# Performance work log

Measured on AMD Instinct MI355X. Metric: run time of the kernel, lower is better.

## Reference

```python
import jax, jax.numpy as jnp
import numpy as np

NUM_GRAPHS = 1024


def setup_inputs() -> dict:
    key = jax.random.key(0)
    k1, k2, k3, k4 = jax.random.split(key, 4)
    N, D = 1000000, 128
    node_embeddings = jax.random.normal(k1, (N, D), dtype=jnp.float32)
    batch_idx = jnp.sort(jax.random.randint(k2, (N,), 0, NUM_GRAPHS))
    # gate MLP params (Linear(D,D) -> ReLU -> Linear(D,1)), scaled like kaiming-ish init
    W1 = jax.random.normal(k3, (D, D), dtype=jnp.float32) / np.sqrt(D)
    b1 = jnp.zeros((D,), dtype=jnp.float32)
    W2 = jax.random.normal(k4, (D, 1), dtype=jnp.float32) / np.sqrt(D)
    b2 = jnp.zeros((1,), dtype=jnp.float32)
    return {"node_embeddings": node_embeddings, "batch_idx": batch_idx,
            "W1": W1, "b1": b1, "W2": W2, "b2": b2}


def reference(node_embeddings, batch_idx, W1, b1, W2, b2):
    # gate = sigmoid(Linear(ReLU(Linear(x))))  -> [N, 1]
    h = jax.nn.relu(node_embeddings @ W1 + b1)          # [N, D]
    gate = jax.nn.sigmoid(h @ W2 + b2)                   # [N, 1]
    gated = gate * node_embeddings                       # [N, D]
    # scatter-sum over batch_idx -> per-graph embedding [B, D]
    graph_embedding = jax.ops.segment_sum(gated, batch_idx, num_segments=NUM_GRAPHS)
    return graph_embedding
```

## Files before the change

### kernel.cpp

```cpp
#include <hip/hip_runtime.h>
#include <stdint.h>

#define D 128
#define TM 64
#define GRID 768
#define NTHREADS 256
#define PPS 17

typedef float f32x4 __attribute__((ext_vector_type(4)));
typedef short s16x8 __attribute__((ext_vector_type(8)));
typedef uint32_t u32x2 __attribute__((ext_vector_type(2)));

__device__ __forceinline__ uint32_t f2bf_u(float f) {
    union { float f; uint32_t u; } v; v.f = f;
    return (v.u + 0x7fffu + ((v.u >> 16) & 1u)) >> 16;
}
__device__ __forceinline__ short f2bf(float f) { return (short)f2bf_u(f); }
__device__ __forceinline__ uint32_t cvt_pk_bf16(float lo, float hi) {
    uint32_t r;
    asm("v_cvt_pk_bf16_f32 %0, %1, %2" : "=v"(r) : "v"(lo), "v"(hi));
    return r;
}

__global__ __launch_bounds__(NTHREADS, 3)
void gate_agg_kernel(const float* __restrict__ X,
                     const int* __restrict__ bidx,
                     const float* __restrict__ W1,
                     const float* __restrict__ b1,
                     const float* __restrict__ W2,
                     const float* __restrict__ b2,
                     float* __restrict__ out,
                     int NT)
{
    __shared__ short xtile[TM * D];
    __shared__ float pp[64 * PPS];
    __shared__ u32x2 gidL[TM];
    __shared__ int   idxL[TM];

    const int tid = threadIdx.x;
    const int l = tid & 63;
    const int w = tid >> 6;
    const int l15 = l & 15;
    const int lk = l >> 4;

    s16x8 bfr[2][4];
    #pragma unroll
    for (int j = 0; j < 2; ++j) {
        const int n = (2 * w + j) * 16 + l15;
        #pragma unroll
        for (int kt = 0; kt < 4; ++kt) {
            #pragma unroll
            for (int e = 0; e < 8; ++e)
                bfr[j][kt][e] = f2bf(W1[(kt * 32 + lk * 8 + e) * D + n]);
        }
    }
    float b1v[2], w2v[2];
    #pragma unroll
    for (int j = 0; j < 2; ++j) {
        b1v[j] = b1[(2 * w + j) * 16 + l15];
        w2v[j] = W2[(2 * w + j) * 16 + l15];
    }
    const float b2s = b2[0];

    const int q = NT / GRID, rem = NT % GRID;
    int t0, t1;
    if ((int)blockIdx.x < rem) { t0 = blockIdx.x * (q + 1); t1 = t0 + q + 1; }
    else { t0 = rem * (q + 1) + ((int)blockIdx.x - rem) * q; t1 = t0 + q; }

    const int cc = tid & 31;
    const int rg = tid >> 5;
    float acc3[4] = {0.f, 0.f, 0.f, 0.f};
    int cur = -1;

    f32x4 v[8];
    int ridx = 0;
    if (t0 < t1) {
        const float* xg = X + (size_t)t0 * TM * D;
        #pragma unroll
        for (int j = 0; j < 8; ++j)
            v[j] = *(const f32x4*)(xg + (size_t)(j * 256 + tid) * 4);
        if (tid < TM) ridx = bidx[(size_t)t0 * TM + tid];
    }

    for (int t = t0; t < t1; ++t) {
        #pragma unroll
        for (int j = 0; j < 8; ++j) {
            int qc = j * 256 + tid;
            int row = qc >> 5, cq = qc & 31;
            int c2 = cq >> 1, h = cq & 1;
            u32x2 wv;
            wv[0] = cvt_pk_bf16(v[j][0], v[j][1]);
            wv[1] = cvt_pk_bf16(v[j][2], v[j][3]);
            *(u32x2*)((char*)xtile + row * 256 + ((c2 ^ (row & 15)) << 4) + h * 8) = wv;
        }
        if (tid < TM) idxL[tid] = ridx;
        __syncthreads();

        if (t + 1 < t1) {
            const float* xg = X + (size_t)(t + 1) * TM * D;
            #pragma unroll
            for (int j = 0; j < 8; ++j)
                v[j] = *(const f32x4*)(xg + (size_t)(j * 256 + tid) * 4);
            if (tid < TM) ridx = bidx[(size_t)(t + 1) * TM + tid];
        }

        f32x4 acc[4][2];
        #pragma unroll
        for (int rf = 0; rf < 4; ++rf) { acc[rf][0] = (f32x4)0.f; acc[rf][1] = (f32x4)0.f; }

        #pragma unroll
        for (int kt = 0; kt < 4; ++kt) {
            const int kc = kt * 4 + lk;
            #pragma unroll
            for (int rf = 0; rf < 4; ++rf) {
                const int R = rf * 16 + l15;
                s16x8 a = *(const s16x8*)((const char*)xtile + R * 256 + ((kc ^ l15) << 4));
                acc[rf][0] = __builtin_amdgcn_mfma_f32_16x16x32_bf16(a, bfr[0][kt], acc[rf][0], 0, 0, 0);
                acc[rf][1] = __builtin_amdgcn_mfma_f32_16x16x32_bf16(a, bfr[1][kt], acc[rf][1], 0, 0, 0);
            }
        }

        #pragma unroll
        for (int rf = 0; rf < 4; ++rf) {
            float pr[4];
            #pragma unroll
            for (int r = 0; r < 4; ++r) {
                float s = 0.f;
                #pragma unroll
                for (int j = 0; j < 2; ++j) {
                    float h = acc[rf][j][r] + b1v[j];
                    h = fmaxf(h, 0.f);
                    s = fmaf(h, w2v[j], s);
                }
                s += __shfl_xor(s, 1, 64);
                s += __shfl_xor(s, 2, 64);
                pr[r] = s;
            }
            float val = pr[0];
            val = ((l & 3) == 1) ? pr[1] : val;
            val = ((l & 3) == 2) ? pr[2] : val;
            val = ((l & 3) == 3) ? pr[3] : val;
            pp[(rf * 16 + lk * 4 + (l & 3)) * PPS + w * 4 + ((l >> 2) & 3)] = val;
        }
        __syncthreads();

        if (tid < TM) {
            float s = 0.f;
            #pragma unroll
            for (int c = 0; c < 16; ++c) s += pp[tid * PPS + c];
            float g = 1.f / (1.f + __expf(-(s + b2s)));
            u32x2 gi; gi[0] = __float_as_uint(g); gi[1] = (uint32_t)idxL[tid];
            gidL[tid] = gi;
        }
        __syncthreads();

        #pragma unroll
        for (int rr = 0; rr < 8; ++rr) {
            int r = rg * 8 + rr;
            u32x2 gi = gidL[r];
            int seg = (int)gi[1];
            float g = __uint_as_float(gi[0]);
            if (seg != cur) {
                if (cur >= 0) {
                    #pragma unroll
                    for (int i = 0; i < 4; ++i)
                        atomicAdd(out + (size_t)cur * D + 4 * cc + i, acc3[i]);
                }
                acc3[0] = acc3[1] = acc3[2] = acc3[3] = 0.f;
                cur = seg;
            }
            u32x2 xw = *(const u32x2*)((const char*)xtile + r * 256 +
                        (((cc >> 1) ^ (r & 15)) << 4) + (cc & 1) * 8);
            float f0 = __uint_as_float(xw[0] << 16);
            float f1 = __uint_as_float(xw[0] & 0xffff0000u);
            float f2 = __uint_as_float(xw[1] << 16);
            float f3 = __uint_as_float(xw[1] & 0xffff0000u);
            acc3[0] = fmaf(g, f0, acc3[0]);
            acc3[1] = fmaf(g, f1, acc3[1]);
            acc3[2] = fmaf(g, f2, acc3[2]);
            acc3[3] = fmaf(g, f3, acc3[3]);
        }
        __syncthreads();
    }
    if (cur >= 0) {
        #pragma unroll
        for (int i = 0; i < 4; ++i)
            atomicAdd(out + (size_t)cur * D + 4 * cc + i, acc3[i]);
    }
}

extern "C" void kernel_launch(void* const* d_in, const int* in_sizes, int n_in,
                              void* d_out, int out_size, void* d_ws, size_t ws_size,
                              hipStream_t stream) {
    const float* X    = (const float*)d_in[0];
    const int*   bidx = (const int*)d_in[1];
    const float* W1   = (const float*)d_in[2];
    const float* b1   = (const float*)d_in[3];
    const float* W2   = (const float*)d_in[4];
    const float* b2   = (const float*)d_in[5];
    float* out = (float*)d_out;

    const int N  = in_sizes[0] / D;
    const int NT = N / TM;

    hipMemsetAsync(d_out, 0, (size_t)out_size * sizeof(float), stream);
    gate_agg_kernel<<<GRID, NTHREADS, 0, stream>>>(X, bidx, W1, b1, W2, b2, out, NT);
}
```

Baseline: 122.0 us.

## Stream fp32 tiles into double-buffered LDS via direct global-to-LDS loads

Replaces the register-staged prefetch and bf16 conversion into shared memory with direct global_load_lds into a double-buffered fp32 LDS tile, converting to bf16 only when forming MFMA operands. The aggregation now reads fp32 from LDS, so it no longer accumulates rounded bf16 values. This frees VGPRs, drops one barrier per tile and overlaps the next tile's load with compute. The cost is 64 KB of LDS, occupancy lowered to 2 blocks per CU with the grid cut to 512, and raw s_barrier/waitcnt synchronisation that must be ordered correctly.

Result: slower. 133.7 us (+9.6%).

```diff
diff --git a/kernel.cpp b/kernel.cpp
--- a/kernel.cpp
+++ b/kernel.cpp
@@ -3,13 +3,14 @@
 
 #define D 128
 #define TM 64
-#define GRID 768
+#define GRID 512
 #define NTHREADS 256
 #define PPS 17
 
 typedef float f32x4 __attribute__((ext_vector_type(4)));
 typedef short s16x8 __attribute__((ext_vector_type(8)));
 typedef uint32_t u32x2 __attribute__((ext_vector_type(2)));
+typedef uint32_t u32x4 __attribute__((ext_vector_type(4)));
 
 __device__ __forceinline__ uint32_t f2bf_u(float f) {
     union { float f; uint32_t u; } v; v.f = f;
@@ -21,8 +22,13 @@
     asm("v_cvt_pk_bf16_f32 %0, %1, %2" : "=v"(r) : "v"(lo), "v"(hi));
     return r;
 }
-
-__global__ __launch_bounds__(NTHREADS, 3)
+__device__ __forceinline__ void gld16(const float* g, float* l) {
+    __builtin_amdgcn_global_load_lds(
+        (const __attribute__((address_space(1))) void*)g,
+        (__attribute__((address_space(3))) void*)l, 16, 0, 0);
+}
+
+__global__ __launch_bounds__(NTHREADS, 2)
 void gate_agg_kernel(const float* __restrict__ X,
                      const int* __restrict__ bidx,
                      const float* __restrict__ W1,
@@ -32,10 +38,9 @@
                      float* __restrict__ out,
                      int NT)
 {
-    __shared__ short xtile[TM * D];
+    __shared__ float fbuf[2][TM * D];
     __shared__ float pp[64 * PPS];
     __shared__ u32x2 gidL[TM];
-    __shared__ int   idxL[TM];
 
     const int tid = threadIdx.x;
     const int l = tid & 63;
@@ -72,37 +77,38 @@
     float acc3[4] = {0.f, 0.f, 0.f, 0.f};
     int cur = -1;
 
-    f32x4 v[8];
-    int ridx = 0;
+    const int lrh = l >> 5;
+    const int lch = l & 31;
+
     if (t0 < t1) {
         const float* xg = X + (size_t)t0 * TM * D;
         #pragma unroll
-        for (int j = 0; j < 8; ++j)
-            v[j] = *(const f32x4*)(xg + (size_t)(j * 256 + tid) * 4);
-        if (tid < TM) ridx = bidx[(size_t)t0 * TM + tid];
-    }
-
-    for (int t = t0; t < t1; ++t) {
-        #pragma unroll
-        for (int j = 0; j < 8; ++j) {
-            int qc = j * 256 + tid;
-            int row = qc >> 5, cq = qc & 31;
-            int c2 = cq >> 1, h = cq & 1;
-            u32x2 wv;
-            wv[0] = cvt_pk_bf16(v[j][0], v[j][1]);
-            wv[1] = cvt_pk_bf16(v[j][2], v[j][3]);
-            *(u32x2*)((char*)xtile + row * 256 + ((c2 ^ (row & 15)) << 4) + h * 8) = wv;
-        }
-        if (tid < TM) idxL[tid] = ridx;
-        __syncthreads();
+        for (int i = 0; i < 8; ++i) {
+            const int r = 16 * w + 2 * i + lrh;
+            gld16(xg + r * D + ((lch ^ (r & 15)) << 2),
+                  &fbuf[0][(16 * w + 2 * i) * D]);
+        }
+    }
+
+    int cb = 0;
+    for (int t = t0; t < t1; ++t, cb ^= 1) {
+        asm volatile("s_waitcnt vmcnt(0)" ::: "memory");
+        __builtin_amdgcn_s_barrier();
+
+        int ridx = 0;
+        if (tid < TM) ridx = bidx[(size_t)t * TM + tid];
 
         if (t + 1 < t1) {
             const float* xg = X + (size_t)(t + 1) * TM * D;
             #pragma unroll
-            for (int j = 0; j < 8; ++j)
-                v[j] = *(const f32x4*)(xg + (size_t)(j * 256 + tid) * 4);
-            if (tid < TM) ridx = bidx[(size_t)(t + 1) * TM + tid];
-        }
+            for (int i = 0; i < 8; ++i) {
+                const int r = 16 * w + 2 * i + lrh;
+                gld16(xg + r * D + ((lch ^ (r & 15)) << 2),
+                      &fbuf[cb ^ 1][(16 * w + 2 * i) * D]);
+            }
+        }
+
+        const float* fb = fbuf[cb];
 
         f32x4 acc[4][2];
         #pragma unroll
@@ -110,13 +116,20 @@
 
         #pragma unroll
         for (int kt = 0; kt < 4; ++kt) {
-            const int kc = kt * 4 + lk;
+            const int kc2 = (kt * 4 + lk) * 2;
             #pragma unroll
             for (int rf = 0; rf < 4; ++rf) {
                 const int R = rf * 16 + l15;
-                s16x8 a = *(const s16x8*)((const char*)xtile + R * 256 + ((kc ^ l15) << 4));
-                acc[rf][0] = __builtin_amdgcn_mfma_f32_16x16x32_bf16(a, bfr[0][kt], acc[rf][0], 0, 0, 0);
-                acc[rf][1] = __builtin_amdgcn_mfma_f32_16x16x32_bf16(a, bfr[1][kt], acc[rf][1], 0, 0, 0);
+                const char* rb = (const char*)fb + R * 512;
+                f32x4 xa = *(const f32x4*)(rb + ((kc2 ^ l15) << 4));
+                f32x4 xb = *(const f32x4*)(rb + (((kc2 + 1) ^ l15) << 4));
+                union { u32x4 u; s16x8 s; } A;
+                A.u[0] = cvt_pk_bf16(xa[0], xa[1]);
+                A.u[1] = cvt_pk_bf16(xa[2], xa[3]);
+                A.u[2] = cvt_pk_bf16(xb[0], xb[1]);
+                A.u[3] = cvt_pk_bf16(xb[2], xb[3]);
+                acc[rf][0] = __builtin_amdgcn_mfma_f32_16x16x32_bf16(A.s, bfr[0][kt], acc[rf][0], 0, 0, 0);
+                acc[rf][1] = __builtin_amdgcn_mfma_f32_16x16x32_bf16(A.s, bfr[1][kt], acc[rf][1], 0, 0, 0);
             }
         }
 
@@ -142,24 +155,26 @@
             val = ((l & 3) == 3) ? pr[3] : val;
             pp[(rf * 16 + lk * 4 + (l & 3)) * PPS + w * 4 + ((l >> 2) & 3)] = val;
         }
-        __syncthreads();
+        asm volatile("s_waitcnt lgkmcnt(0)" ::: "memory");
+        __builtin_amdgcn_s_barrier();
 
         if (tid < TM) {
             float s = 0.f;
             #pragma unroll
             for (int c = 0; c < 16; ++c) s += pp[tid * PPS + c];
             float g = 1.f / (1.f + __expf(-(s + b2s)));
-            u32x2 gi; gi[0] = __float_as_uint(g); gi[1] = (uint32_t)idxL[tid];
+            u32x2 gi; gi[0] = __float_as_uint(g); gi[1] = (uint32_t)ridx;
             gidL[tid] = gi;
         }
-        __syncthreads();
+        asm volatile("s_waitcnt lgkmcnt(0)" ::: "memory");
+        __builtin_amdgcn_s_barrier();
 
         #pragma unroll
         for (int rr = 0; rr < 8; ++rr) {
-            int r = rg * 8 + rr;
+            const int r = rg * 8 + rr;
             u32x2 gi = gidL[r];
-            int seg = (int)gi[1];
-            float g = __uint_as_float(gi[0]);
+            const int seg = (int)gi[1];
+            const float g = __uint_as_float(gi[0]);
             if (seg != cur) {
                 if (cur >= 0) {
                     #pragma unroll
@@ -169,18 +184,12 @@
                 acc3[0] = acc3[1] = acc3[2] = acc3[3] = 0.f;
                 cur = seg;
             }
-            u32x2 xw = *(const u32x2*)((const char*)xtile + r * 256 +
-                        (((cc >> 1) ^ (r & 15)) << 4) + (cc & 1) * 8);
-            float f0 = __uint_as_float(xw[0] << 16);
-            float f1 = __uint_as_float(xw[0] & 0xffff0000u);
-            float f2 = __uint_as_float(xw[1] << 16);
-            float f3 = __uint_as_float(xw[1] & 0xffff0000u);
-            acc3[0] = fmaf(g, f0, acc3[0]);
-            acc3[1] = fmaf(g, f1, acc3[1]);
-            acc3[2] = fmaf(g, f2, acc3[2]);
-            acc3[3] = fmaf(g, f3, acc3[3]);
-        }
-        __syncthreads();
+            f32x4 xw = *(const f32x4*)((const char*)fb + r * 512 + ((cc ^ (r & 15)) << 4));
+            acc3[0] = fmaf(g, xw[0], acc3[0]);
+            acc3[1] = fmaf(g, xw[1], acc3[1]);
+            acc3[2] = fmaf(g, xw[2], acc3[2]);
+            acc3[3] = fmaf(g, xw[3], acc3[3]);
+        }
     }
     if (cur >= 0) {
         #pragma unroll
```
